# Kernel tuning notes

Hardware: AMD Instinct MI355X
Metric: run time of the kernel (lower is better)

The kernel has to match this reference:

```python
import jax, jax.numpy as jnp
import numpy as np

NUM_HEADS = 16

def setup_inputs() -> dict:
    key = jax.random.key(0)
    ks = jax.random.split(key, 8)
    T, B, E = 2048, 2, 1024
    s = 1.0 / np.sqrt(E)
    return {
        "query": jax.random.normal(ks[0], (T, B, E), jnp.float32),
        "key": jax.random.normal(ks[1], (T, B, E), jnp.float32),
        "value": jax.random.normal(ks[2], (T, B, E), jnp.float32),
        "Wq": jax.random.normal(ks[3], (E, E), jnp.float32) * s,
        "bq": jnp.zeros((E,), jnp.float32),
        "Wk": jax.random.normal(ks[4], (E, E), jnp.float32) * s,
        "bk": jnp.zeros((E,), jnp.float32),
        "Wv": jax.random.normal(ks[5], (E, E), jnp.float32) * s,
        "bv": jnp.zeros((E,), jnp.float32),
        "Wo": jax.random.normal(ks[6], (E, E), jnp.float32) * s,
        "bo": jnp.zeros((E,), jnp.float32),
    }

def reference(query, key, value, Wq, bq, Wk, bk, Wv, bv, Wo, bo):
    T, B, E = query.shape
    S = key.shape[0]
    H = NUM_HEADS
    hd = E // H
    scaling = float(hd) ** -0.5
    # linear projections (torch Linear: x @ W.T + b)
    q = (query @ Wq.T + bq).reshape(T, B, H, hd)
    k = (key @ Wk.T + bk).reshape(S, B, H, hd)
    v = (value @ Wv.T + bv).reshape(S, B, H, hd)
    # scores: (B, H, T, S)
    scores = jnp.einsum('tbhd,sbhd->bhts', q, k) * scaling
    attn = jax.nn.softmax(scores, axis=-1)  # dropout p=0
    # weighted sum: (T, B, H, hd) -> (T, B, E)
    out = jnp.einsum('bhts,sbhd->tbhd', attn, v).reshape(T, B, E)
    out = out @ Wo.T + bo
    # averaged attention weights over heads: (B, T, S)
    avg_w = attn.mean(axis=1)
    return (out, avg_w)
```

## Files before the change

### kernel.cpp

```cpp
#include <hip/hip_runtime.h>
#include <hip/hip_bf16.h>
#include <stdint.h>

#define HN 16
#define TT 2048
#define BBATCH 2
#define EE 1024
#define HD 64
#define MM 4096

#define SCALEQ 0.18033688011112042f

typedef __attribute__((ext_vector_type(8))) __bf16 bfrag;
typedef __attribute__((ext_vector_type(4))) float f32x4;
typedef __attribute__((ext_vector_type(4))) short s16x4;

__device__ __forceinline__ void gll16(const void* g, void* lds) {
  __builtin_amdgcn_global_load_lds(
      (const __attribute__((address_space(1))) void*)g,
      (__attribute__((address_space(3))) void*)lds, 16, 0, 0);
}

__device__ __forceinline__ f32x4 mfma_bf16(bfrag a, bfrag b, f32x4 c) {
  return __builtin_amdgcn_mfma_f32_16x16x32_bf16(a, b, c, 0, 0, 0);
}

__device__ __forceinline__ const bfrag* fragp(const __bf16* base, int row, int e) {
  return (const bfrag*)(base + row * 64 + ((((e >> 3) ^ row) & 7) << 3));
}
__device__ __forceinline__ void stage8(const __bf16* grow0, int gstride,
                                       __bf16* tile, int r0, int lane) {
  const int rr = lane >> 3;
  const int cl = (lane & 7) ^ rr;
  gll16(grow0 + (size_t)(r0 + rr) * gstride + cl * 8, tile + r0 * 64);
}

struct CvtArgs {
  const float* src[7];
  __bf16* dst[7];
  int n4[7];
};

__global__ __launch_bounds__(256) void cvt_all(CvtArgs a) {
  const int z = blockIdx.z;
  const int i = blockIdx.x * 256 + threadIdx.x;
  if (i < a.n4[z]) {
    float4 v = ((const float4*)a.src[z])[i];
    struct alignas(8) B4 { __bf16 a0, a1, a2, a3; };
    B4 o = {(__bf16)v.x, (__bf16)v.y, (__bf16)v.z, (__bf16)v.w};
    ((B4*)a.dst[z])[i] = o;
  }
}

template <int MT>
__device__ __forceinline__ void gemm2(const __bf16* __restrict__ X,
                                      const __bf16* __restrict__ W,
                                      const float* __restrict__ bias,
                                      void* __restrict__ out, int mode,
                                      float scale, int m0, int n0,
                                      __bf16* As0, __bf16* As1,
                                      __bf16* Bs0, __bf16* Bs1) {
  const int tid = threadIdx.x, lane = tid & 63, w = tid >> 6;
  const int wm = w >> 1, wn = w & 1;
  const int quad = lane >> 4, l16 = lane & 15;
  constexpr int FM = MT / 32;

  auto stageAB = [&](int buf, int k0) {
    __bf16* A = buf ? As1 : As0;
    __bf16* B = buf ? Bs1 : Bs0;
    #pragma unroll
    for (int c = 0; c < FM; ++c)
      stage8(X + (size_t)m0 * EE + k0, EE, A, w * (MT / 4) + c * 8, lane);
    #pragma unroll
    for (int c = 0; c < 4; ++c)
      stage8(W + (size_t)n0 * EE + k0, EE, B, w * 32 + c * 8, lane);
  };

  stageAB(0, 0);

  f32x4 acc[FM][4] = {};

  for (int it = 0; it < EE / 64; ++it) {
    const int cur = it & 1;
    __syncthreads();
    if (it + 1 < EE / 64) stageAB(1 - cur, (it + 1) * 64);

    const __bf16* A = cur ? As1 : As0;
    const __bf16* B = cur ? Bs1 : Bs0;
    #pragma unroll
    for (int ks = 0; ks < 2; ++ks) {
      bfrag a[FM], b[4];
      #pragma unroll
      for (int f = 0; f < FM; ++f)
        a[f] = *fragp(A, wm * (MT / 2) + f * 16 + l16, ks * 32 + quad * 8);
      #pragma unroll
      for (int f = 0; f < 4; ++f)
        b[f] = *fragp(B, wn * 64 + f * 16 + l16, ks * 32 + quad * 8);
      #pragma unroll
      for (int fm = 0; fm < FM; ++fm)
        #pragma unroll
        for (int fn = 0; fn < 4; ++fn)
          acc[fm][fn] = mfma_bf16(a[fm], b[fn], acc[fm][fn]);
    }
  }

  float bv[4];
  #pragma unroll
  for (int fn = 0; fn < 4; ++fn) bv[fn] = bias[n0 + wn * 64 + fn * 16 + l16];

  #pragma unroll
  for (int fm = 0; fm < FM; ++fm) {
    #pragma unroll
    for (int r = 0; r < 4; ++r) {
      const int gm = m0 + wm * (MT / 2) + fm * 16 + quad * 4 + r;
      #pragma unroll
      for (int fn = 0; fn < 4; ++fn) {
        const int gn = n0 + wn * 64 + fn * 16 + l16;
        const float v = (acc[fm][fn][r] + bv[fn]) * scale;
        if (mode == 0) {
          const int t = gm >> 1, bb = gm & 1, h = gn >> 6, d = gn & 63;
          ((__bf16*)out)[(((size_t)(bb * HN + h)) * TT + t) * HD + d] = (__bf16)v;
        } else if (mode == 2) {
          const int s = gm >> 1, bb = gm & 1, h = gn >> 6, d = gn & 63;
          ((__bf16*)out)[(((size_t)(bb * HN + h)) * HD + d) * TT + s] = (__bf16)v;
        } else {
          ((float*)out)[(size_t)gm * EE + gn] = v;
        }
      }
    }
  }
}

__global__ __launch_bounds__(256, 2) void gemm_qkv(
    const __bf16* __restrict__ xq, const __bf16* __restrict__ xk,
    const __bf16* __restrict__ xv, const __bf16* __restrict__ wq,
    const __bf16* __restrict__ wk, const __bf16* __restrict__ wv,
    const float* __restrict__ bq, const float* __restrict__ bk,
    const float* __restrict__ bv, __bf16* __restrict__ qo,
    __bf16* __restrict__ ko, __bf16* __restrict__ vo) {
  __shared__ __bf16 As[2][128 * 64];
  __shared__ __bf16 Bs[2][128 * 64];
  const int bx = blockIdx.x;
  const int m = bx & 31, n = (bx >> 5) & 7, z = bx >> 8;
  const __bf16 *X, *W;
  const float* bias;
  __bf16* out;
  int mode;
  float scale;
  if (z == 0)      { X = xq; W = wq; bias = bq; out = qo; mode = 0; scale = SCALEQ; }
  else if (z == 1) { X = xk; W = wk; bias = bk; out = ko; mode = 0; scale = 1.0f; }
  else             { X = xv; W = wv; bias = bv; out = vo; mode = 2; scale = 1.0f; }
  gemm2<128>(X, W, bias, out, mode, scale, m * 128, n * 128,
             As[0], As[1], Bs[0], Bs[1]);
}

__global__ __launch_bounds__(256, 2) void gemm_o(const __bf16* __restrict__ X,
                                                 const __bf16* __restrict__ W,
                                                 const float* __restrict__ bias,
                                                 float* __restrict__ out) {
  __shared__ __bf16 As[2][64 * 64];
  __shared__ __bf16 Bs[2][128 * 64];
  const int bx = blockIdx.x;
  const int m = bx & 63, n = bx >> 6;
  gemm2<64>(X, W, bias, out, 3, 1.0f, m * 64, n * 128,
            As[0], As[1], Bs[0], Bs[1]);
}

__global__ __launch_bounds__(256, 2) void attn_fwd(const __bf16* __restrict__ qb,
                                                   const __bf16* __restrict__ kb,
                                                   const __bf16* __restrict__ vtb,
                                                   __bf16* __restrict__ ob,
                                                   float* __restrict__ linv_ws) {
  union Sh {
    __bf16 kv[2][2][2][64 * 64];
    float om[2][64 * 64];
  };
  __shared__ Sh sm;
  __shared__ float Lsum[2][128];
  __shared__ float LinvS[128];

  const int tid = threadIdx.x, lane = tid & 63, w = tid >> 6;
  const int p = w >> 1, tw = w & 1;
  const int quad = lane >> 4, l16 = lane & 15;

  const int bx = blockIdx.x;
  const int xcd = bx & 7, slot = bx >> 3;
  const int bhi = xcd * 4 + (slot >> 4);
  const int t0 = (slot & 15) * 128;
  const int b = bhi >> 4, h = bhi & 15;
  const size_t bh = (size_t)(b * HN + h);

  const __bf16* qbase = qb + (bh * TT + t0) * HD;
  const __bf16* kbase = kb + bh * TT * HD;
  const __bf16* vbase = vtb + bh * HD * TT;
  const int sBase = p * 1024;

  #pragma unroll
  for (int c = 0; c < 4; ++c) {
    stage8(kbase + (size_t)sBase * HD, HD, sm.kv[p][0][0], tw * 32 + c * 8, lane);
    stage8(vbase + sBase, TT, sm.kv[p][1][0], tw * 32 + c * 8, lane);
  }

  bfrag qf[4][2];
  #pragma unroll
  for (int fn = 0; fn < 4; ++fn)
    #pragma unroll
    for (int ks = 0; ks < 2; ++ks)
      qf[fn][ks] = *(const bfrag*)(qbase +
          (size_t)(tw * 64 + fn * 16 + l16) * HD + ks * 32 + quad * 8);

  bfrag ones;
  {
    union { short s[8]; bfrag v; } u;
    #pragma unroll
    for (int i = 0; i < 8; ++i) u.s[i] = 0x3F80;
    ones = u.v;
  }

  f32x4 oacc[4][4] = {};
  f32x4 lacc[4] = {};

  for (int it = 0; it < 16; ++it) {
    const int cur = it & 1;
    __syncthreads();
    if (it + 1 < 16) {
      const int s1 = sBase + (it + 1) * 64;
      #pragma unroll
      for (int c = 0; c < 4; ++c) {
        stage8(kbase + (size_t)s1 * HD, HD, sm.kv[p][0][1 - cur], tw * 32 + c * 8, lane);
        stage8(vbase + s1, TT, sm.kv[p][1][1 - cur], tw * 32 + c * 8, lane);
      }
    }

    f32x4 sacc[4][4] = {};
    #pragma unroll
    for (int ks = 0; ks < 2; ++ks) {
      bfrag kf[4];
      #pragma unroll
      for (int fm = 0; fm < 4; ++fm)
        kf[fm] = *fragp(sm.kv[p][0][cur], fm * 16 + l16, ks * 32 + quad * 8);
      #pragma unroll
      for (int fm = 0; fm < 4; ++fm)
        #pragma unroll
        for (int fn = 0; fn < 4; ++fn)
          sacc[fm][fn] = mfma_bf16(kf[fm], qf[fn][ks], sacc[fm][fn]);
    }

    union PB { __bf16 hh[8]; bfrag v; } pb[2][4];
    #pragma unroll
    for (int fm = 0; fm < 4; ++fm)
      #pragma unroll
      for (int fn = 0; fn < 4; ++fn) {
        const float p0 = __builtin_amdgcn_exp2f(sacc[fm][fn][0]);
        const float p1 = __builtin_amdgcn_exp2f(sacc[fm][fn][1]);
        const float p2 = __builtin_amdgcn_exp2f(sacc[fm][fn][2]);
        const float p3 = __builtin_amdgcn_exp2f(sacc[fm][fn][3]);
        const int hb = (fm & 1) * 4;
        pb[fm >> 1][fn].hh[hb + 0] = (__bf16)p0;
        pb[fm >> 1][fn].hh[hb + 1] = (__bf16)p1;
        pb[fm >> 1][fn].hh[hb + 2] = (__bf16)p2;
        pb[fm >> 1][fn].hh[hb + 3] = (__bf16)p3;
      }

    #pragma unroll
    for (int ks = 0; ks < 2; ++ks) {
      bfrag vf[4];
      #pragma unroll
      for (int fm = 0; fm < 4; ++fm) {
        const __bf16* base = sm.kv[p][1][cur] + (fm * 16 + l16) * 64;
        const int sw = l16 & 7, qh = quad >> 1, qo = (quad & 1) * 4;
        union VF { s16x4 q[2]; bfrag v; } u;
        u.q[0] = *(const s16x4*)(base + (((ks * 4 + qh) ^ sw) << 3) + qo);
        u.q[1] = *(const s16x4*)(base + (((ks * 4 + 2 + qh) ^ sw) << 3) + qo);
        vf[fm] = u.v;
      }
      #pragma unroll
      for (int fn = 0; fn < 4; ++fn)
        lacc[fn] = mfma_bf16(ones, pb[ks][fn].v, lacc[fn]);
      #pragma unroll
      for (int fm = 0; fm < 4; ++fm)
        #pragma unroll
        for (int fn = 0; fn < 4; ++fn)
          oacc[fm][fn] = mfma_bf16(vf[fm], pb[ks][fn].v, oacc[fm][fn]);
    }
  }

  if (quad == 0)
    #pragma unroll
    for (int fn = 0; fn < 4; ++fn)
      Lsum[p][tw * 64 + fn * 16 + l16] = lacc[fn][0];

  __syncthreads();

  if (p == 1) {
    #pragma unroll
    for (int fm = 0; fm < 4; ++fm)
      #pragma unroll
      for (int fn = 0; fn < 4; ++fn)
        #pragma unroll
        for (int r = 0; r < 4; ++r)
          sm.om[tw][(fm * 16 + quad * 4 + r) * 64 + fn * 16 + l16] = oacc[fm][fn][r];
  }
  if (tid < 128) {
    const float linv = 1.0f / (Lsum[0][tid] + Lsum[1][tid]);
    LinvS[tid] = linv;
    linv_ws[bh * TT + t0 + tid] = linv;
  }
  __syncthreads();

  if (p == 0) {
    float li[4];
    #pragma unroll
    for (int fn = 0; fn < 4; ++fn) li[fn] = LinvS[tw * 64 + fn * 16 + l16];
    #pragma unroll
    for (int fm = 0; fm < 4; ++fm)
      #pragma unroll
      for (int fn = 0; fn < 4; ++fn) {
        const int t = t0 + tw * 64 + fn * 16 + l16;
        struct alignas(8) B4 { __bf16 a0, a1, a2, a3; };
        B4 o;
        __bf16* op = &o.a0;
        #pragma unroll
        for (int r = 0; r < 4; ++r) {
          const float v = (oacc[fm][fn][r] +
              sm.om[tw][(fm * 16 + quad * 4 + r) * 64 + fn * 16 + l16]) * li[fn];
          op[r] = (__bf16)v;
        }
        *(B4*)(ob + ((size_t)t * BBATCH + b) * EE + h * HD + fm * 16 + quad * 4) = o;
      }
  }
}

__global__ __launch_bounds__(256, 2) void avg_attn(const __bf16* __restrict__ qb,
                                                   const __bf16* __restrict__ kb,
                                                   const float* __restrict__ linv_ws,
                                                   float* __restrict__ avg_out) {
  __shared__ __bf16 Qs[2][128 * 64];
  __shared__ __bf16 Ks[2][128 * 64];

  const int tid = threadIdx.x, lane = tid & 63, w = tid >> 6;
  const int wm = w >> 1, wn = w & 1;
  const int quad = lane >> 4, l16 = lane & 15;

  const int bx = blockIdx.x;
  const int xcd = bx & 7, slot = bx >> 3;
  const int bti = xcd * 4 + (slot >> 4);
  const int s0 = (slot & 15) * 128;
  const int b = bti >> 4, t0 = (bti & 15) * 128;

  const __bf16* qt = qb + (((size_t)b * HN) * TT + t0) * HD;
  const __bf16* kt = kb + (((size_t)b * HN) * TT + s0) * HD;
  const float* lrow0 = linv_ws + ((size_t)b * HN) * TT + t0 + wm * 64;

  #pragma unroll
  for (int c = 0; c < 4; ++c) {
    stage8(qt, HD, Qs[0], w * 32 + c * 8, lane);
    stage8(kt, HD, Ks[0], w * 32 + c * 8, lane);
  }

  f32x4 aacc[4][4] = {};

  for (int h = 0; h < HN; ++h) {
    const int cur = h & 1;
    __syncthreads();
    if (h + 1 < HN) {
      const __bf16* qn = qt + (size_t)(h + 1) * TT * HD;
      const __bf16* kn = kt + (size_t)(h + 1) * TT * HD;
      #pragma unroll
      for (int c = 0; c < 4; ++c) {
        stage8(qn, HD, Qs[1 - cur], w * 32 + c * 8, lane);
        stage8(kn, HD, Ks[1 - cur], w * 32 + c * 8, lane);
      }
    }

    f32x4 sacc[4][4] = {};
    #pragma unroll
    for (int ks = 0; ks < 2; ++ks) {
      bfrag qf4[4], kf4[4];
      #pragma unroll
      for (int f = 0; f < 4; ++f)
        qf4[f] = *fragp(Qs[cur], wm * 64 + f * 16 + l16, ks * 32 + quad * 8);
      #pragma unroll
      for (int f = 0; f < 4; ++f)
        kf4[f] = *fragp(Ks[cur], wn * 64 + f * 16 + l16, ks * 32 + quad * 8);
      #pragma unroll
      for (int fm = 0; fm < 4; ++fm)
        #pragma unroll
        for (int fn = 0; fn < 4; ++fn)
          sacc[fm][fn] = mfma_bf16(qf4[fm], kf4[fn], sacc[fm][fn]);
    }

    const float* lr = lrow0 + (size_t)h * TT;
    f32x4 lvv[4];
    #pragma unroll
    for (int fm = 0; fm < 4; ++fm)
      lvv[fm] = *(const f32x4*)(lr + fm * 16 + quad * 4);

    #pragma unroll
    for (int fm = 0; fm < 4; ++fm)
      #pragma unroll
      for (int fn = 0; fn < 4; ++fn)
        #pragma unroll
        for (int r = 0; r < 4; ++r)
          aacc[fm][fn][r] += __builtin_amdgcn_exp2f(sacc[fm][fn][r]) * lvv[fm][r];
  }

  const float invh = 1.0f / (float)HN;
  #pragma unroll
  for (int fm = 0; fm < 4; ++fm)
    #pragma unroll
    for (int r = 0; r < 4; ++r) {
      const int t = t0 + wm * 64 + fm * 16 + quad * 4 + r;
      #pragma unroll
      for (int fn = 0; fn < 4; ++fn) {
        const int s = s0 + wn * 64 + fn * 16 + l16;
        avg_out[((size_t)b * TT + t) * TT + s] = aacc[fm][fn][r] * invh;
      }
    }
}

extern "C" void kernel_launch(void* const* d_in, const int* in_sizes, int n_in,
                              void* d_out, int out_size, void* d_ws, size_t ws_size,
                              hipStream_t stream) {
  (void)in_sizes; (void)n_in; (void)out_size; (void)ws_size;
  const float* query = (const float*)d_in[0];
  const float* key   = (const float*)d_in[1];
  const float* value = (const float*)d_in[2];
  const float* Wq = (const float*)d_in[3];
  const float* bq = (const float*)d_in[4];
  const float* Wk = (const float*)d_in[5];
  const float* bk = (const float*)d_in[6];
  const float* Wv = (const float*)d_in[7];
  const float* bv = (const float*)d_in[8];
  const float* Wo = (const float*)d_in[9];
  const float* bo = (const float*)d_in[10];

  char* ws = (char*)d_ws;
  size_t off = 0;
  auto wsalloc = [&](size_t bytes) -> void* {
    void* p = ws + off;
    off += (bytes + 255) & ~(size_t)255;
    return p;
  };
  const size_t XE = (size_t)MM * EE;
  const size_t WE = (size_t)EE * EE;
  __bf16* xq   = (__bf16*)wsalloc(XE * 2);
  __bf16* xk   = (__bf16*)wsalloc(XE * 2);
  __bf16* xv   = (__bf16*)wsalloc(XE * 2);
  __bf16* wqb  = (__bf16*)wsalloc(WE * 2);
  __bf16* wkb  = (__bf16*)wsalloc(WE * 2);
  __bf16* wvb  = (__bf16*)wsalloc(WE * 2);
  __bf16* wob  = (__bf16*)wsalloc(WE * 2);
  __bf16* qbuf = (__bf16*)wsalloc(XE * 2);
  __bf16* kbuf = (__bf16*)wsalloc(XE * 2);
  __bf16* vtbuf= (__bf16*)wsalloc(XE * 2);
  __bf16* obuf = (__bf16*)wsalloc(XE * 2);
  float* linv  = (float*)wsalloc((size_t)BBATCH * HN * TT * 4);

  CvtArgs ca;
  ca.src[0] = query; ca.dst[0] = xq;  ca.n4[0] = (int)(XE / 4);
  ca.src[1] = key;   ca.dst[1] = xk;  ca.n4[1] = (int)(XE / 4);
  ca.src[2] = value; ca.dst[2] = xv;  ca.n4[2] = (int)(XE / 4);
  ca.src[3] = Wq;    ca.dst[3] = wqb; ca.n4[3] = (int)(WE / 4);
  ca.src[4] = Wk;    ca.dst[4] = wkb; ca.n4[4] = (int)(WE / 4);
  ca.src[5] = Wv;    ca.dst[5] = wvb; ca.n4[5] = (int)(WE / 4);
  ca.src[6] = Wo;    ca.dst[6] = wob; ca.n4[6] = (int)(WE / 4);
  cvt_all<<<dim3(4096, 1, 7), 256, 0, stream>>>(ca);

  gemm_qkv<<<dim3(768), 256, 0, stream>>>(xq, xk, xv, wqb, wkb, wvb,
                                          bq, bk, bv, qbuf, kbuf, vtbuf);

  attn_fwd<<<dim3(512), 256, 0, stream>>>(qbuf, kbuf, vtbuf, obuf, linv);

  float* avg_out = (float*)d_out + (size_t)TT * BBATCH * EE;
  avg_attn<<<dim3(512), 256, 0, stream>>>(qbuf, kbuf, linv, avg_out);

  gemm_o<<<dim3(512), 256, 0, stream>>>(obuf, wob, bo, (float*)d_out);
}
```

Measured before the change: 258.7 us.

## Use 256x256 8-wave pipelined QKV GEMM and fuse avg-attn with output GEMM

Replaces the 128x128 QKV projection GEMM with a 256x256-tile, 512-thread kernel. It interleaves LDS fragment reads, async global-to-LDS staging and MFMA quadrants, using explicit barriers, waitcnt gates and setprio to overlap loads with math. It also merges the averaged-attention kernel and the output projection GEMM into one launch, with block ranges dispatched to each body and a shared LDS union. This cuts launch overhead and lets the two independent tail workloads co-schedule on the CUs. The larger GEMM tile raises LDS use (128KB) and register pressure, and with only 192 blocks occupancy and load balance may suffer.

```diff
diff --git a/kernel.cpp b/kernel.cpp
--- a/kernel.cpp
+++ b/kernel.cpp
@@ -131,17 +131,21 @@
   }
 }
 
-__global__ __launch_bounds__(256, 2) void gemm_qkv(
+__global__ __launch_bounds__(512, 2) void gemm_qkv8(
     const __bf16* __restrict__ xq, const __bf16* __restrict__ xk,
     const __bf16* __restrict__ xv, const __bf16* __restrict__ wq,
     const __bf16* __restrict__ wk, const __bf16* __restrict__ wv,
     const float* __restrict__ bq, const float* __restrict__ bk,
     const float* __restrict__ bv, __bf16* __restrict__ qo,
     __bf16* __restrict__ ko, __bf16* __restrict__ vo) {
-  __shared__ __bf16 As[2][128 * 64];
-  __shared__ __bf16 Bs[2][128 * 64];
+  __shared__ __bf16 As[2][256 * 64];
+  __shared__ __bf16 Bs[2][256 * 64];
+  const int tid = threadIdx.x, lane = tid & 63, w = tid >> 6;
+  const int wm = w >> 2, wn = w & 3;
+  const int quad = lane >> 4, l16 = lane & 15;
+
   const int bx = blockIdx.x;
-  const int m = bx & 31, n = (bx >> 5) & 7, z = bx >> 8;
+  const int m = bx & 15, n = (bx >> 4) & 3, z = bx >> 6;
   const __bf16 *X, *W;
   const float* bias;
   __bf16* out;
@@ -150,20 +154,138 @@
   if (z == 0)      { X = xq; W = wq; bias = bq; out = qo; mode = 0; scale = SCALEQ; }
   else if (z == 1) { X = xk; W = wk; bias = bk; out = ko; mode = 0; scale = 1.0f; }
   else             { X = xv; W = wv; bias = bv; out = vo; mode = 2; scale = 1.0f; }
-  gemm2<128>(X, W, bias, out, mode, scale, m * 128, n * 128,
-             As[0], As[1], Bs[0], Bs[1]);
-}
-
-__global__ __launch_bounds__(256, 2) void gemm_o(const __bf16* __restrict__ X,
-                                                 const __bf16* __restrict__ W,
-                                                 const float* __restrict__ bias,
-                                                 float* __restrict__ out) {
-  __shared__ __bf16 As[2][64 * 64];
-  __shared__ __bf16 Bs[2][128 * 64];
-  const int bx = blockIdx.x;
-  const int m = bx & 63, n = bx >> 6;
-  gemm2<64>(X, W, bias, out, 3, 1.0f, m * 64, n * 128,
-            As[0], As[1], Bs[0], Bs[1]);
+  const int m0 = m * 256, n0 = n * 256;
+  const __bf16* Ag = X + (size_t)m0 * EE;
+  const __bf16* Bg = W + (size_t)n0 * EE;
+  __bf16* As0 = As[0]; __bf16* As1 = As[1];
+  __bf16* Bs0 = Bs[0]; __bf16* Bs1 = Bs[1];
+
+  auto stageHalf = [&](const __bf16* g, __bf16* tile, int r0) {
+    #pragma unroll
+    for (int c = 0; c < 2; ++c)
+      stage8(g, EE, tile, r0 + w * 16 + c * 8, lane);
+  };
+
+  stageHalf(Ag, As0, 0);      stageHalf(Ag, As0, 128);
+  stageHalf(Bg, Bs0, 0);      stageHalf(Bg, Bs0, 128);
+  stageHalf(Ag + 64, As1, 0); stageHalf(Ag + 64, As1, 128);
+  asm volatile("s_waitcnt vmcnt(4)" ::: "memory");
+  __builtin_amdgcn_s_barrier();
+
+  f32x4 acc[8][4] = {};
+
+  auto quad4 = [&](const __bf16* Ac, const __bf16* Bc,
+                   const __bf16* g1, __bf16* l1, bool do1,
+                   const __bf16* g4, __bf16* l4, bool do4, int gate) {
+    bfrag a[4][2], b0[2][2], b1[2][2];
+    #pragma unroll
+    for (int f = 0; f < 4; ++f)
+      #pragma unroll
+      for (int ks = 0; ks < 2; ++ks)
+        a[f][ks] = *fragp(Ac, wm * 128 + f * 16 + l16, ks * 32 + quad * 8);
+    #pragma unroll
+    for (int f = 0; f < 2; ++f)
+      #pragma unroll
+      for (int ks = 0; ks < 2; ++ks)
+        b0[f][ks] = *fragp(Bc, wn * 64 + f * 16 + l16, ks * 32 + quad * 8);
+    if (do1) { stageHalf(g1, l1, 0); stageHalf(g1, l1, 128); }
+    __builtin_amdgcn_s_barrier();
+    asm volatile("s_waitcnt lgkmcnt(0)" ::: "memory");
+    __builtin_amdgcn_sched_barrier(0);
+    __builtin_amdgcn_s_setprio(1);
+    #pragma unroll
+    for (int ks = 0; ks < 2; ++ks)
+      #pragma unroll
+      for (int f = 0; f < 4; ++f)
+        #pragma unroll
+        for (int fn = 0; fn < 2; ++fn)
+          acc[f][fn] = mfma_bf16(a[f][ks], b0[fn][ks], acc[f][fn]);
+    __builtin_amdgcn_s_setprio(0);
+    __builtin_amdgcn_s_barrier();
+    #pragma unroll
+    for (int f = 0; f < 2; ++f)
+      #pragma unroll
+      for (int ks = 0; ks < 2; ++ks)
+        b1[f][ks] = *fragp(Bc, wn * 64 + (2 + f) * 16 + l16, ks * 32 + quad * 8);
+    __builtin_amdgcn_s_barrier();
+    asm volatile("s_waitcnt lgkmcnt(0)" ::: "memory");
+    __builtin_amdgcn_sched_barrier(0);
+    __builtin_amdgcn_s_setprio(1);
+    #pragma unroll
+    for (int ks = 0; ks < 2; ++ks)
+      #pragma unroll
+      for (int f = 0; f < 4; ++f)
+        #pragma unroll
+        for (int fn = 0; fn < 2; ++fn)
+          acc[f][2 + fn] = mfma_bf16(a[f][ks], b1[fn][ks], acc[f][2 + fn]);
+    __builtin_amdgcn_s_setprio(0);
+    __builtin_amdgcn_s_barrier();
+    #pragma unroll
+    for (int f = 0; f < 4; ++f)
+      #pragma unroll
+      for (int ks = 0; ks < 2; ++ks)
+        a[f][ks] = *fragp(Ac, wm * 128 + (4 + f) * 16 + l16, ks * 32 + quad * 8);
+    __builtin_amdgcn_s_barrier();
+    asm volatile("s_waitcnt lgkmcnt(0)" ::: "memory");
+    __builtin_amdgcn_sched_barrier(0);
+    __builtin_amdgcn_s_setprio(1);
+    #pragma unroll
+    for (int ks = 0; ks < 2; ++ks)
+      #pragma unroll
+      for (int f = 0; f < 4; ++f)
+        #pragma unroll
+        for (int fn = 0; fn < 2; ++fn)
+          acc[4 + f][2 + fn] = mfma_bf16(a[f][ks], b1[fn][ks], acc[4 + f][2 + fn]);
+    __builtin_amdgcn_s_setprio(0);
+    __builtin_amdgcn_s_barrier();
+    if (do4) { stageHalf(g4, l4, 0); stageHalf(g4, l4, 128); }
+    if (gate == 0)      asm volatile("s_waitcnt vmcnt(4)" ::: "memory");
+    else if (gate == 1) asm volatile("s_waitcnt vmcnt(0)" ::: "memory");
+    __builtin_amdgcn_s_barrier();
+    __builtin_amdgcn_s_setprio(1);
+    #pragma unroll
+    for (int ks = 0; ks < 2; ++ks)
+      #pragma unroll
+      for (int f = 0; f < 4; ++f)
+        #pragma unroll
+        for (int fn = 0; fn < 2; ++fn)
+          acc[4 + f][fn] = mfma_bf16(a[f][ks], b0[fn][ks], acc[4 + f][fn]);
+    __builtin_amdgcn_s_setprio(0);
+    __builtin_amdgcn_s_barrier();
+  };
+
+  for (int i = 0; i < 8; ++i) {
+    const int k0 = i * 128;
+    const bool nl = (i < 7);
+    quad4(As0, Bs0, Bg + k0 + 64, Bs1, true,
+          Ag + k0 + 128, As0, nl, nl ? 0 : 1);
+    quad4(As1, Bs1, Bg + k0 + 128, Bs0, nl,
+          Ag + k0 + 192, As1, nl, nl ? 0 : 2);
+  }
+
+  float bvv[4];
+  #pragma unroll
+  for (int fn = 0; fn < 4; ++fn) bvv[fn] = bias[n0 + wn * 64 + fn * 16 + l16];
+
+  #pragma unroll
+  for (int fm = 0; fm < 8; ++fm) {
+    #pragma unroll
+    for (int r = 0; r < 4; ++r) {
+      const int gm = m0 + wm * 128 + fm * 16 + quad * 4 + r;
+      #pragma unroll
+      for (int fn = 0; fn < 4; ++fn) {
+        const int gn = n0 + wn * 64 + fn * 16 + l16;
+        const float v = (acc[fm][fn][r] + bvv[fn]) * scale;
+        if (mode == 0) {
+          const int t = gm >> 1, bb = gm & 1, h = gn >> 6, d = gn & 63;
+          out[(((size_t)(bb * HN + h)) * TT + t) * HD + d] = (__bf16)v;
+        } else {
+          const int s = gm >> 1, bb = gm & 1, h = gn >> 6, d = gn & 63;
+          out[(((size_t)(bb * HN + h)) * HD + d) * TT + s] = (__bf16)v;
+        }
+      }
+    }
+  }
 }
 
 __global__ __launch_bounds__(256, 2) void attn_fwd(const __bf16* __restrict__ qb,
@@ -331,18 +453,16 @@
   }
 }
 
-__global__ __launch_bounds__(256, 2) void avg_attn(const __bf16* __restrict__ qb,
-                                                   const __bf16* __restrict__ kb,
-                                                   const float* __restrict__ linv_ws,
-                                                   float* __restrict__ avg_out) {
-  __shared__ __bf16 Qs[2][128 * 64];
-  __shared__ __bf16 Ks[2][128 * 64];
-
+__device__ __forceinline__ void avg_body(const __bf16* __restrict__ qb,
+                                         const __bf16* __restrict__ kb,
+                                         const float* __restrict__ linv_ws,
+                                         float* __restrict__ avg_out, int bx,
+                                         __bf16* Qs0, __bf16* Qs1,
+                                         __bf16* Ks0, __bf16* Ks1) {
   const int tid = threadIdx.x, lane = tid & 63, w = tid >> 6;
   const int wm = w >> 1, wn = w & 1;
   const int quad = lane >> 4, l16 = lane & 15;
 
-  const int bx = blockIdx.x;
   const int xcd = bx & 7, slot = bx >> 3;
   const int bti = xcd * 4 + (slot >> 4);
   const int s0 = (slot & 15) * 128;
@@ -354,8 +474,8 @@
 
   #pragma unroll
   for (int c = 0; c < 4; ++c) {
-    stage8(qt, HD, Qs[0], w * 32 + c * 8, lane);
-    stage8(kt, HD, Ks[0], w * 32 + c * 8, lane);
+    stage8(qt, HD, Qs0, w * 32 + c * 8, lane);
+    stage8(kt, HD, Ks0, w * 32 + c * 8, lane);
   }
 
   f32x4 aacc[4][4] = {};
@@ -366,23 +486,27 @@
     if (h + 1 < HN) {
       const __bf16* qn = qt + (size_t)(h + 1) * TT * HD;
       const __bf16* kn = kt + (size_t)(h + 1) * TT * HD;
+      __bf16* Qn = cur ? Qs0 : Qs1;
+      __bf16* Kn = cur ? Ks0 : Ks1;
       #pragma unroll
       for (int c = 0; c < 4; ++c) {
-        stage8(qn, HD, Qs[1 - cur], w * 32 + c * 8, lane);
-        stage8(kn, HD, Ks[1 - cur], w * 32 + c * 8, lane);
-      }
-    }
-
+        stage8(qn, HD, Qn, w * 32 + c * 8, lane);
+        stage8(kn, HD, Kn, w * 32 + c * 8, lane);
+      }
+    }
+
+    const __bf16* Qc = cur ? Qs1 : Qs0;
+    const __bf16* Kc = cur ? Ks1 : Ks0;
     f32x4 sacc[4][4] = {};
     #pragma unroll
     for (int ks = 0; ks < 2; ++ks) {
       bfrag qf4[4], kf4[4];
       #pragma unroll
       for (int f = 0; f < 4; ++f)
-        qf4[f] = *fragp(Qs[cur], wm * 64 + f * 16 + l16, ks * 32 + quad * 8);
+        qf4[f] = *fragp(Qc, wm * 64 + f * 16 + l16, ks * 32 + quad * 8);
       #pragma unroll
       for (int f = 0; f < 4; ++f)
-        kf4[f] = *fragp(Ks[cur], wn * 64 + f * 16 + l16, ks * 32 + quad * 8);
+        kf4[f] = *fragp(Kc, wn * 64 + f * 16 + l16, ks * 32 + quad * 8);
       #pragma unroll
       for (int fm = 0; fm < 4; ++fm)
         #pragma unroll
@@ -417,6 +541,28 @@
         avg_out[((size_t)b * TT + t) * TT + s] = aacc[fm][fn][r] * invh;
       }
     }
+}
+
+struct TailAvg { __bf16 Qs[2][128 * 64]; __bf16 Ks[2][128 * 64]; };
+struct TailGo  { __bf16 As[2][64 * 64];  __bf16 Bs[2][128 * 64]; };
+union TailSh { TailAvg a; TailGo g; };
+
+__global__ __launch_bounds__(256, 2) void tail_fused(
+    const __bf16* __restrict__ qb, const __bf16* __restrict__ kb,
+    const float* __restrict__ linv_ws, float* __restrict__ avg_out,
+    const __bf16* __restrict__ ob, const __bf16* __restrict__ wo,
+    const float* __restrict__ bo, float* __restrict__ out) {
+  __shared__ TailSh sh;
+  const int bx = blockIdx.x;
+  if (bx < 512) {
+    avg_body(qb, kb, linv_ws, avg_out, bx,
+             sh.a.Qs[0], sh.a.Qs[1], sh.a.Ks[0], sh.a.Ks[1]);
+  } else {
+    const int b2 = bx - 512;
+    const int m = b2 & 63, n = b2 >> 6;
+    gemm2<64>(ob, wo, bo, out, 3, 1.0f, m * 64, n * 128,
+              sh.g.As[0], sh.g.As[1], sh.g.Bs[0], sh.g.Bs[1]);
+  }
 }
 
 extern "C" void kernel_launch(void* const* d_in, const int* in_sizes, int n_in,
@@ -467,13 +613,12 @@
   ca.src[6] = Wo;    ca.dst[6] = wob; ca.n4[6] = (int)(WE / 4);
   cvt_all<<<dim3(4096, 1, 7), 256, 0, stream>>>(ca);
 
-  gemm_qkv<<<dim3(768), 256, 0, stream>>>(xq, xk, xv, wqb, wkb, wvb,
-                                          bq, bk, bv, qbuf, kbuf, vtbuf);
+  gemm_qkv8<<<dim3(192), 512, 0, stream>>>(xq, xk, xv, wqb, wkb, wvb,
+                                           bq, bk, bv, qbuf, kbuf, vtbuf);
 
   attn_fwd<<<dim3(512), 256, 0, stream>>>(qbuf, kbuf, vtbuf, obuf, linv);
 
   float* avg_out = (float*)d_out + (size_t)TT * BBATCH * EE;
-  avg_attn<<<dim3(512), 256, 0, stream>>>(qbuf, kbuf, linv, avg_out);
-
-  gemm_o<<<dim3(512), 256, 0, stream>>>(obuf, wob, bo, (float*)d_out);
-}
+  tail_fused<<<dim3(1024), 256, 0, stream>>>(qbuf, kbuf, linv, avg_out,
+                                             obuf, wob, bo, (float*)d_out);
+}
```

Result: no change. 260.3 us (+0.6%).
